# Kernel optimization log

Hardware: AMD Instinct MI355X
Metric: run time of the kernel (lower is better)

## Reference

```python
import jax, jax.numpy as jnp
import numpy as np

E, K, D, H = 8, 2, 1024, 2048   # num_experts, top_k, dim, ffn_dim
B, S = 1, 1024                   # batch, seq


def setup_inputs() -> dict:
    key = jax.random.key(0)
    k0, k1, k2, k3, k4 = jax.random.split(key, 5)
    sD = 1.0 / np.sqrt(D)
    sH = 1.0 / np.sqrt(H)
    return {
        "hidden_states": jax.random.normal(k0, (B, S, D), jnp.float32),
        "gate_w": jax.random.normal(k1, (E, D), jnp.float32) * sD,
        "w1": jax.random.normal(k2, (E, D, H), jnp.float32) * sD,
        "w2": jax.random.normal(k3, (E, H, D), jnp.float32) * sH,
        "w3": jax.random.normal(k4, (E, D, H), jnp.float32) * sD,
    }


def _grouped_swiglu(x_sorted, counts, w1, w2, w3):
    """Grouped expert SwiGLU over tokens sorted by expert id.

    x_sorted: [T, D] tokens grouped contiguously by expert (expert 0 first).
    counts:   [E] number of tokens per expert (sums to T).
    """
    if hasattr(jax.lax, "ragged_dot"):
        gs = counts.astype(jnp.int32)
        h = jax.nn.silu(jax.lax.ragged_dot(x_sorted, w1, gs)) * jax.lax.ragged_dot(x_sorted, w3, gs)
        return jax.lax.ragged_dot(h, w2, gs)
    # Fallback: per-expert masked GEMM (same math; zeros pass through silu*mul).
    pos = jnp.arange(x_sorted.shape[0])
    eid = jnp.searchsorted(jnp.cumsum(counts), pos, side="right")  # expert of each sorted token
    out = jnp.zeros((x_sorted.shape[0], w2.shape[-1]), x_sorted.dtype)
    for e in range(w1.shape[0]):
        xm = jnp.where((eid == e)[:, None], x_sorted, 0.0)
        he = jax.nn.silu(xm @ w1[e]) * (xm @ w3[e])
        out = out + he @ w2[e]
    return out


def reference(hidden_states, gate_w, w1, w2, w3):
    x = hidden_states.reshape(-1, D)                      # [N, D]
    N = x.shape[0]
    # --- router: softmax over experts, then top-k ---
    scores = jax.nn.softmax(x @ gate_w.T, axis=-1)        # [N, E]
    top_scores, sel = jax.lax.top_k(scores, K)            # [N, K]
    # flatten slot-major so flat_idx % N == token id (matches `% num_tokens`)
    sel_flat = sel.T.reshape(-1)                          # [K*N]
    scores_flat = top_scores.T.reshape(-1)                # [K*N]
    # --- reorder: stable sort by expert id ---
    order = jnp.argsort(sel_flat, stable=True)            # [K*N]
    tok_sorted = order % N                                # original token per routed slot
    scores_sorted = scores_flat[order]
    counts = jnp.bincount(sel_flat, length=E)             # tokens per expert
    # --- dispatch (ep_size=1: all-to-all is identity) + grouped expert GEMM ---
    x_sorted = x[tok_sorted]                              # [K*N, D]
    y = _grouped_swiglu(x_sorted, counts, w1, w2, w3)     # [K*N, D]
    # --- weighted scatter-combine ---
    weighted = y * scores_sorted[:, None]
    out = jnp.zeros((N, D), x.dtype).at[tok_sorted].add(weighted)
    return out.reshape(hidden_states.shape)
```

## Files before the change

### kernel.cpp

```cpp
#include <hip/hip_runtime.h>
#include <hip/hip_bf16.h>
#include <math.h>

#define NE 8
#define DD 1024
#define HH 2048
#define NTOK 1024
#define NSLOT 2048
#define NSLOTP 3072

typedef short short8v __attribute__((ext_vector_type(8)));
typedef float f32x4 __attribute__((ext_vector_type(4)));

static __device__ __forceinline__ unsigned short f2bf(float f) {
  union { __hip_bfloat16 h; unsigned short u; } c;
  c.h = __float2bfloat16(f);
  return c.u;
}

static __device__ __forceinline__ int sigma(int n) {
  return ((n >> 1) & 3) ^ ((n >> 3) & 1);
}

static __device__ __forceinline__ short8v pk8(const float* q) {
  short8v v;
#pragma unroll
  for (int i = 0; i < 8; ++i) v[i] = (short)f2bf(q[i]);
  return v;
}

__global__ __launch_bounds__(64) void krouter(const float* __restrict__ x,
                                              const float* __restrict__ gw,
                                              int* __restrict__ e_sel,
                                              float* __restrict__ w_sel) {
  int n = blockIdx.x;
  int lane = threadIdx.x;
  const float4* xr = (const float4*)(x + (size_t)n * DD);
  const float4* gr = (const float4*)gw;
  float acc[NE];
#pragma unroll
  for (int e = 0; e < NE; ++e) acc[e] = 0.f;
#pragma unroll
  for (int i = 0; i < 4; ++i) {
    float4 xv = xr[lane + i * 64];
#pragma unroll
    for (int e = 0; e < NE; ++e) {
      float4 gv = gr[e * 256 + lane + i * 64];
      acc[e] += xv.x * gv.x + xv.y * gv.y + xv.z * gv.z + xv.w * gv.w;
    }
  }
#pragma unroll
  for (int e = 0; e < NE; ++e)
#pragma unroll
    for (int off = 32; off > 0; off >>= 1) acc[e] += __shfl_xor(acc[e], off);
  if (lane == 0) {
    float m = acc[0];
#pragma unroll
    for (int e = 1; e < NE; ++e) m = fmaxf(m, acc[e]);
    float p[NE];
    float z = 0.f;
#pragma unroll
    for (int e = 0; e < NE; ++e) { p[e] = expf(acc[e] - m); z += p[e]; }
    float inv = 1.f / z;
    int e1 = 0;
#pragma unroll
    for (int e = 1; e < NE; ++e) if (acc[e] > acc[e1]) e1 = e;
    int e2 = (e1 == 0) ? 1 : 0;
#pragma unroll
    for (int e = 0; e < NE; ++e) if (e != e1 && acc[e] > acc[e2]) e2 = e;
    e_sel[n] = e1;         w_sel[n] = p[e1] * inv;
    e_sel[NTOK + n] = e2;  w_sel[NTOK + n] = p[e2] * inv;
  }
}

__global__ __launch_bounds__(256) void kbuild(const int* __restrict__ e_sel,
                                              const float* __restrict__ w_sel,
                                              int* __restrict__ tok,
                                              float* __restrict__ wgt,
                                              int* __restrict__ meta) {
  __shared__ int sc[NE], scur[NE];
  int t = threadIdx.x;
  if (t < NE) sc[t] = 0;
  __syncthreads();
  for (int s = t; s < NSLOTP; s += 256) tok[s] = -1;
  for (int s = t; s < NSLOT; s += 256) atomicAdd(&sc[e_sel[s]], 1);
  __syncthreads();
  if (t == 0) {
    int run = 0, i64 = 0, i128 = 0;
    for (int e = 0; e < NE; ++e) {
      meta[8 + e] = run; scur[e] = run;
      meta[e] = sc[e];
      int nm = (sc[e] + 127) >> 7;
      for (int m = 0; m < nm; ++m) {
        meta[128 + i128] = e; meta[152 + i128] = m; ++i128;
      }
      for (int m = 0; m < 2 * nm; ++m) {
        meta[32 + i64] = e; meta[80 + i64] = m; ++i64;
      }
      run += nm << 7;
    }
    meta[16] = i64; meta[17] = i128;
  }
  __syncthreads();
  for (int s = t; s < NSLOT; s += 256) {
    int e = e_sel[s];
    int pos = atomicAdd(&scur[e], 1);
    tok[pos] = s & (NTOK - 1);
    wgt[pos] = w_sel[s];
  }
}

__global__ __launch_bounds__(256) void kgather(const float* __restrict__ x,
                                               const int* __restrict__ tok,
                                               unsigned short* __restrict__ xg) {
  int tid = threadIdx.x;
  int row = blockIdx.x * 2 + (tid >> 7);
  int g = tid & 127;
  int t = tok[row];
  int pos = (g & 3) ^ ((row >> 1) & 3);
  char* dst = (char*)xg + (size_t)row * 2048 + (g >> 2) * 64 + (pos << 4);
  short8v v = {0, 0, 0, 0, 0, 0, 0, 0};
  if (t >= 0) {
    const float* src = x + (size_t)t * DD + g * 8;
    float q[8];
#pragma unroll
    for (int i = 0; i < 8; ++i) q[i] = src[i];
    v = pk8(q);
  }
  *(short8v*)dst = v;
}

__global__ __launch_bounds__(256, 3) void kgemm13(
    const unsigned short* __restrict__ xg, const float* __restrict__ w1,
    const float* __restrict__ w3, unsigned short* __restrict__ hws,
    const int* __restrict__ meta) {
  __shared__ __align__(16) char smem[16384];
  char* ldsB = smem;
  int vt = blockIdx.y;
  if (vt >= meta[17]) return;
  int e = meta[128 + vt], mt = meta[152 + vt];
  int n0 = blockIdx.x * 64;
  int abase = meta[8 + e] + mt * 128;
  int tid = threadIdx.x, l = tid & 63, w = tid >> 6;
  int wm = w & 1, wn = w >> 1;

  int bn = tid & 63, kb = tid >> 6;
  const float* pb1 = w1 + (size_t)e * DD * HH + (size_t)(kb * 8) * HH + n0 + bn;
  const float* pb3 = w3 + (size_t)e * DD * HH + (size_t)(kb * 8) * HH + n0 + bn;
  int wb = bn * 64 + (((kb ^ sigma(bn)) & 3) << 4);

  const char* pa[4];
#pragma unroll
  for (int mf = 0; mf < 4; ++mf) {
    int r = wm * 64 + mf * 16 + (l & 15);
    pa[mf] = (const char*)xg + (size_t)(abase + r) * 2048 +
             ((((l >> 4) ^ (r >> 1)) & 3) << 4);
  }
  int boff[2];
#pragma unroll
  for (int nf = 0; nf < 2; ++nf) {
    int n = wn * 32 + nf * 16 + (l & 15);
    boff[nf] = n * 64 + ((((l >> 4) ^ sigma(n)) & 3) << 4);
  }

  f32x4 accg[4][2], accu[4][2];
#pragma unroll
  for (int i = 0; i < 4; ++i)
#pragma unroll
    for (int j = 0; j < 2; ++j) {
      accg[i][j] = (f32x4){0.f, 0.f, 0.f, 0.f};
      accu[i][j] = (f32x4){0.f, 0.f, 0.f, 0.f};
    }

  float q1[2][8], q3[2][8];
  short8v a[4];
#pragma unroll
  for (int r = 0; r < 8; ++r) {
    q1[0][r] = pb1[(size_t)r * HH];
    q3[0][r] = pb3[(size_t)r * HH];
    q1[1][r] = pb1[(size_t)(32 + r) * HH];
    q3[1][r] = pb3[(size_t)(32 + r) * HH];
  }
#pragma unroll
  for (int mf = 0; mf < 4; ++mf) a[mf] = *(const short8v*)(pa[mf]);
  *(short8v*)(ldsB + wb) = pk8(q1[0]);
  *(short8v*)(ldsB + 4096 + wb) = pk8(q3[0]);
#pragma unroll
  for (int r = 0; r < 8; ++r) {
    q1[0][r] = pb1[(size_t)(64 + r) * HH];
    q3[0][r] = pb3[(size_t)(64 + r) * HH];
  }
  __syncthreads();

#define STEP13(S, P)                                                           \
  {                                                                            \
    if ((S) < 31) {                                                            \
      char* d = ldsB + (((P) ^ 1) << 13);                                      \
      *(short8v*)(d + wb) = pk8(q1[(P) ^ 1]);                                  \
      *(short8v*)(d + 4096 + wb) = pk8(q3[(P) ^ 1]);                           \
    }                                                                          \
    if ((S) < 29) {                                                            \
      const float* s1 = pb1 + (size_t)((S) + 3) * 32 * HH;                     \
      const float* s3 = pb3 + (size_t)((S) + 3) * 32 * HH;                     \
      _Pragma("unroll") for (int r = 0; r < 8; ++r) {                          \
        q1[(P) ^ 1][r] = s1[(size_t)r * HH];                                   \
        q3[(P) ^ 1][r] = s3[(size_t)r * HH];                                   \
      }                                                                        \
    }                                                                          \
    short8v b1f[2], b3f[2];                                                    \
    _Pragma("unroll") for (int nf = 0; nf < 2; ++nf) {                         \
      b1f[nf] = *(const short8v*)(ldsB + ((P) << 13) + boff[nf]);              \
      b3f[nf] = *(const short8v*)(ldsB + ((P) << 13) + 4096 + boff[nf]);       \
    }                                                                          \
    _Pragma("unroll") for (int nf = 0; nf < 2; ++nf)                           \
        _Pragma("unroll") for (int mf = 0; mf < 4; ++mf) {                     \
      accg[mf][nf] = __builtin_amdgcn_mfma_f32_16x16x32_bf16(                  \
          a[mf], b1f[nf], accg[mf][nf], 0, 0, 0);                              \
      accu[mf][nf] = __builtin_amdgcn_mfma_f32_16x16x32_bf16(                  \
          a[mf], b3f[nf], accu[mf][nf], 0, 0, 0);                              \
    }                                                                          \
    if ((S) < 31) {                                                           \
      _Pragma("unroll") for (int mf = 0; mf < 4; ++mf)                         \
          a[mf] = *(const short8v*)(pa[mf] + ((S) + 1) * 64);                  \
    }                                                                          \
    __syncthreads();                                                           \
  }

  for (int ss = 0; ss < 16; ++ss) {
    int s0 = 2 * ss;
    STEP13(s0, 0);
    STEP13(s0 + 1, 1);
  }
#undef STEP13

  unsigned short* hl = (unsigned short*)smem;
#pragma unroll
  for (int mf = 0; mf < 4; ++mf)
#pragma unroll
    for (int nf = 0; nf < 2; ++nf)
#pragma unroll
      for (int rr = 0; rr < 4; ++rr) {
        int row = wm * 64 + mf * 16 + ((l >> 4) << 2) + rr;
        int col = wn * 32 + nf * 16 + (l & 15);
        float gv = accg[mf][nf][rr], uv = accu[mf][nf][rr];
        hl[row * 64 + col] = f2bf((gv / (1.f + __expf(-gv))) * uv);
      }
  __syncthreads();
#pragma unroll
  for (int p = 0; p < 4; ++p) {
    int idx = p * 256 + tid;
    int row = idx >> 3, g = idx & 7;
    int dp = abase + row;
    size_t db = (size_t)dp * 4096 + (size_t)n0 * 2 + (g >> 2) * 64 +
                ((size_t)((g & 3) ^ ((dp >> 1) & 3)) << 4);
    *(short8v*)((char*)hws + db) =
        *(const short8v*)((const char*)hl + row * 128 + (g << 4));
  }
}

__global__ __launch_bounds__(256, 4) void kgemm2(
    const unsigned short* __restrict__ hws, const float* __restrict__ w2,
    float* __restrict__ out, const int* __restrict__ tok,
    const float* __restrict__ wgt, const int* __restrict__ meta) {
  __shared__ __align__(16) char smem[8192];
  char* ldsB = smem;
  int vt = blockIdx.y;
  if (vt >= meta[17]) return;
  int e = meta[128 + vt], mt = meta[152 + vt];
  int n0 = blockIdx.x * 64;
  int kz = blockIdx.z;
  int mbase = meta[8 + e] + mt * 128;
  int rem = meta[e] - mt * 128;
  int tid = threadIdx.x, l = tid & 63, w = tid >> 6;
  int wm = w & 1, wn = w >> 1;

  int bn = tid & 63, kb = tid >> 6;
  const float* pb = w2 + (size_t)e * HH * DD +
                    (size_t)(kz * 1024 + kb * 8) * DD + n0 + bn;
  int wb = bn * 64 + (((kb ^ sigma(bn)) & 3) << 4);

  const char* pa[4];
#pragma unroll
  for (int mf = 0; mf < 4; ++mf) {
    int r = wm * 64 + mf * 16 + (l & 15);
    pa[mf] = (const char*)hws + (size_t)(mbase + r) * 4096 + kz * 2048 +
             ((((l >> 4) ^ (r >> 1)) & 3) << 4);
  }
  int boff[2];
#pragma unroll
  for (int nf = 0; nf < 2; ++nf) {
    int n = wn * 32 + nf * 16 + (l & 15);
    boff[nf] = n * 64 + ((((l >> 4) ^ sigma(n)) & 3) << 4);
  }

  f32x4 acc[4][2];
#pragma unroll
  for (int i = 0; i < 4; ++i)
#pragma unroll
    for (int j = 0; j < 2; ++j) acc[i][j] = (f32x4){0.f, 0.f, 0.f, 0.f};

  float q[2][8];
  short8v a[4];
#pragma unroll
  for (int r = 0; r < 8; ++r) {
    q[0][r] = pb[(size_t)r * DD];
    q[1][r] = pb[(size_t)(32 + r) * DD];
  }
#pragma unroll
  for (int mf = 0; mf < 4; ++mf) a[mf] = *(const short8v*)(pa[mf]);
  *(short8v*)(ldsB + wb) = pk8(q[0]);
#pragma unroll
  for (int r = 0; r < 8; ++r) q[0][r] = pb[(size_t)(64 + r) * DD];
  __syncthreads();

#define STEP2(S, P)                                                            \
  {                                                                            \
    if ((S) < 31) {                                                            \
      *(short8v*)(ldsB + (((P) ^ 1) << 12) + wb) = pk8(q[(P) ^ 1]);            \
    }                                                                          \
    if ((S) < 29) {                                                            \
      const float* sp = pb + (size_t)((S) + 3) * 32 * DD;                      \
      _Pragma("unroll") for (int r = 0; r < 8; ++r)                            \
          q[(P) ^ 1][r] = sp[(size_t)r * DD];                                  \
    }                                                                          \
    short8v bf[2];                                                             \
    _Pragma("unroll") for (int nf = 0; nf < 2; ++nf)                           \
        bf[nf] = *(const short8v*)(ldsB + ((P) << 12) + boff[nf]);             \
    _Pragma("unroll") for (int nf = 0; nf < 2; ++nf)                           \
        _Pragma("unroll") for (int mf = 0; mf < 4; ++mf)                       \
            acc[mf][nf] = __builtin_amdgcn_mfma_f32_16x16x32_bf16(             \
                a[mf], bf[nf], acc[mf][nf], 0, 0, 0);                          \
    if ((S) < 31) {                                                           \
      _Pragma("unroll") for (int mf = 0; mf < 4; ++mf)                         \
          a[mf] = *(const short8v*)(pa[mf] + ((S) + 1) * 64);                  \
    }                                                                          \
    __syncthreads();                                                           \
  }

  for (int ss = 0; ss < 16; ++ss) {
    int s0 = 2 * ss;
    STEP2(s0, 0);
    STEP2(s0 + 1, 1);
  }
#undef STEP2

#pragma unroll
  for (int mf = 0; mf < 4; ++mf)
#pragma unroll
    for (int rr = 0; rr < 4; ++rr) {
      int row = wm * 64 + mf * 16 + ((l >> 4) << 2) + rr;
      if (row < rem) {
        int t = tok[mbase + row];
        float wt = wgt[mbase + row];
#pragma unroll
        for (int nf = 0; nf < 2; ++nf)
          atomicAdd(out + (size_t)t * DD + n0 + wn * 32 + nf * 16 + (l & 15),
                    wt * acc[mf][nf][rr]);
      }
    }
}

extern "C" void kernel_launch(void* const* d_in, const int* in_sizes, int n_in,
                              void* d_out, int out_size, void* d_ws, size_t ws_size,
                              hipStream_t stream) {
  const float* x  = (const float*)d_in[0];
  const float* gw = (const float*)d_in[1];
  const float* w1 = (const float*)d_in[2];
  const float* w2 = (const float*)d_in[3];
  const float* w3 = (const float*)d_in[4];
  float* out = (float*)d_out;
  char* ws = (char*)d_ws;
  const size_t MB = 1024 * 1024;
  if (ws_size < 24 * MB) return;

  unsigned short* xg  = (unsigned short*)(ws);
  unsigned short* hws = (unsigned short*)(ws + 6 * MB);
  char* mb = ws + 20 * MB;
  int*   e_sel  = (int*)mb;
  float* w_sel  = (float*)(mb + 8192);
  int*   tok    = (int*)(mb + 16384);
  float* wgt    = (float*)(mb + 16384 + 12288);
  int*   meta   = (int*)(mb + 16384 + 24576);

  hipMemsetAsync(out, 0, (size_t)out_size * sizeof(float), stream);
  krouter<<<dim3(NTOK), 64, 0, stream>>>(x, gw, e_sel, w_sel);
  kbuild<<<1, 256, 0, stream>>>(e_sel, w_sel, tok, wgt, meta);
  kgather<<<dim3(NSLOTP / 2), 256, 0, stream>>>(x, tok, xg);
  kgemm13<<<dim3(32, 24), 256, 0, stream>>>(xg, w1, w3, hws, meta);
  kgemm2<<<dim3(16, 24, 2), 256, 0, stream>>>(hws, w2, out, tok, wgt, meta);
}
```

Measured before the change: 119.4 us.

## Load expert weights directly into registers per wave, dropping LDS staging and barriers

Both expert GEMM kernels stop staging the fp32 weight tiles in shared memory. Each wave now loads its own 16-column slice straight into registers, converts it to bf16 and feeds the MFMAs with a register double buffer, so the per-step __syncthreads disappears. Each wave covers all 128 rows of the tile, and the activation XOR swizzle is removed from the gather and intermediate buffers. The cost is that every wave reloads all A rows (twice the A traffic per wave), register pressure goes up so occupancy is lowered to 2 blocks, and prefetch depth drops to one step.

```diff
diff --git a/kernel.cpp b/kernel.cpp
--- a/kernel.cpp
+++ b/kernel.cpp
@@ -16,10 +16,6 @@
   union { __hip_bfloat16 h; unsigned short u; } c;
   c.h = __float2bfloat16(f);
   return c.u;
-}
-
-static __device__ __forceinline__ int sigma(int n) {
-  return ((n >> 1) & 3) ^ ((n >> 3) & 1);
 }
 
 static __device__ __forceinline__ short8v pk8(const float* q) {
@@ -117,8 +113,7 @@
   int row = blockIdx.x * 2 + (tid >> 7);
   int g = tid & 127;
   int t = tok[row];
-  int pos = (g & 3) ^ ((row >> 1) & 3);
-  char* dst = (char*)xg + (size_t)row * 2048 + (g >> 2) * 64 + (pos << 4);
+  char* dst = (char*)xg + (size_t)row * 2048 + (g << 4);
   short8v v = {0, 0, 0, 0, 0, 0, 0, 0};
   if (t >= 0) {
     const float* src = x + (size_t)t * DD + g * 8;
@@ -130,140 +125,97 @@
   *(short8v*)dst = v;
 }
 
-__global__ __launch_bounds__(256, 3) void kgemm13(
+__global__ __launch_bounds__(256, 2) void kgemm13(
     const unsigned short* __restrict__ xg, const float* __restrict__ w1,
     const float* __restrict__ w3, unsigned short* __restrict__ hws,
     const int* __restrict__ meta) {
   __shared__ __align__(16) char smem[16384];
-  char* ldsB = smem;
   int vt = blockIdx.y;
   if (vt >= meta[17]) return;
   int e = meta[128 + vt], mt = meta[152 + vt];
   int n0 = blockIdx.x * 64;
   int abase = meta[8 + e] + mt * 128;
   int tid = threadIdx.x, l = tid & 63, w = tid >> 6;
-  int wm = w & 1, wn = w >> 1;
-
-  int bn = tid & 63, kb = tid >> 6;
-  const float* pb1 = w1 + (size_t)e * DD * HH + (size_t)(kb * 8) * HH + n0 + bn;
-  const float* pb3 = w3 + (size_t)e * DD * HH + (size_t)(kb * 8) * HH + n0 + bn;
-  int wb = bn * 64 + (((kb ^ sigma(bn)) & 3) << 4);
-
-  const char* pa[4];
-#pragma unroll
-  for (int mf = 0; mf < 4; ++mf) {
-    int r = wm * 64 + mf * 16 + (l & 15);
-    pa[mf] = (const char*)xg + (size_t)(abase + r) * 2048 +
-             ((((l >> 4) ^ (r >> 1)) & 3) << 4);
-  }
-  int boff[2];
-#pragma unroll
-  for (int nf = 0; nf < 2; ++nf) {
-    int n = wn * 32 + nf * 16 + (l & 15);
-    boff[nf] = n * 64 + ((((l >> 4) ^ sigma(n)) & 3) << 4);
-  }
-
-  f32x4 accg[4][2], accu[4][2];
-#pragma unroll
-  for (int i = 0; i < 4; ++i)
-#pragma unroll
-    for (int j = 0; j < 2; ++j) {
-      accg[i][j] = (f32x4){0.f, 0.f, 0.f, 0.f};
-      accu[i][j] = (f32x4){0.f, 0.f, 0.f, 0.f};
-    }
-
-  float q1[2][8], q3[2][8];
-  short8v a[4];
-#pragma unroll
-  for (int r = 0; r < 8; ++r) {
-    q1[0][r] = pb1[(size_t)r * HH];
-    q3[0][r] = pb3[(size_t)r * HH];
-    q1[1][r] = pb1[(size_t)(32 + r) * HH];
-    q3[1][r] = pb3[(size_t)(32 + r) * HH];
-  }
-#pragma unroll
-  for (int mf = 0; mf < 4; ++mf) a[mf] = *(const short8v*)(pa[mf]);
-  *(short8v*)(ldsB + wb) = pk8(q1[0]);
-  *(short8v*)(ldsB + 4096 + wb) = pk8(q3[0]);
-#pragma unroll
-  for (int r = 0; r < 8; ++r) {
-    q1[0][r] = pb1[(size_t)(64 + r) * HH];
-    q3[0][r] = pb3[(size_t)(64 + r) * HH];
-  }
-  __syncthreads();
-
-#define STEP13(S, P)                                                           \
+
+  const char* pa[8];
+#pragma unroll
+  for (int mf = 0; mf < 8; ++mf) {
+    int r = mf * 16 + (l & 15);
+    pa[mf] = (const char*)xg + (size_t)(abase + r) * 2048 + ((l >> 4) << 4);
+  }
+  int ncol = n0 + w * 16 + (l & 15);
+  const float* pb1 = w1 + (size_t)e * DD * HH + (size_t)((l >> 4) * 8) * HH + ncol;
+  const float* pb3 = w3 + (size_t)e * DD * HH + (size_t)((l >> 4) * 8) * HH + ncol;
+
+  f32x4 accg[8], accu[8];
+#pragma unroll
+  for (int i = 0; i < 8; ++i) {
+    accg[i] = (f32x4){0.f, 0.f, 0.f, 0.f};
+    accu[i] = (f32x4){0.f, 0.f, 0.f, 0.f};
+  }
+
+  float q1A[8], q3A[8], q1B[8], q3B[8];
+  short8v aA[8], aB[8];
+#pragma unroll
+  for (int j = 0; j < 8; ++j) {
+    q1A[j] = pb1[(size_t)j * HH];
+    q3A[j] = pb3[(size_t)j * HH];
+  }
+#pragma unroll
+  for (int mf = 0; mf < 8; ++mf) aA[mf] = *(const short8v*)(pa[mf]);
+
+#define STEP13(S, QC1, QC3, AC, QN1, QN3, AN)                                  \
   {                                                                            \
     if ((S) < 31) {                                                            \
-      char* d = ldsB + (((P) ^ 1) << 13);                                      \
-      *(short8v*)(d + wb) = pk8(q1[(P) ^ 1]);                                  \
-      *(short8v*)(d + 4096 + wb) = pk8(q3[(P) ^ 1]);                           \
+      size_t ko = (size_t)((S) + 1) * 32 * HH;                                 \
+      _Pragma("unroll") for (int j = 0; j < 8; ++j) {                          \
+        QN1[j] = pb1[ko + (size_t)j * HH];                                     \
+        QN3[j] = pb3[ko + (size_t)j * HH];                                     \
+      }                                                                        \
+      _Pragma("unroll") for (int mf = 0; mf < 8; ++mf)                         \
+          AN[mf] = *(const short8v*)(pa[mf] + ((S) + 1) * 64);                 \
     }                                                                          \
-    if ((S) < 29) {                                                            \
-      const float* s1 = pb1 + (size_t)((S) + 3) * 32 * HH;                     \
-      const float* s3 = pb3 + (size_t)((S) + 3) * 32 * HH;                     \
-      _Pragma("unroll") for (int r = 0; r < 8; ++r) {                          \
-        q1[(P) ^ 1][r] = s1[(size_t)r * HH];                                   \
-        q3[(P) ^ 1][r] = s3[(size_t)r * HH];                                   \
-      }                                                                        \
+    short8v b1 = pk8(QC1), b3 = pk8(QC3);                                      \
+    _Pragma("unroll") for (int mf = 0; mf < 8; ++mf) {                         \
+      accg[mf] = __builtin_amdgcn_mfma_f32_16x16x32_bf16(AC[mf], b1,           \
+                                                         accg[mf], 0, 0, 0);   \
+      accu[mf] = __builtin_amdgcn_mfma_f32_16x16x32_bf16(AC[mf], b3,           \
+                                                         accu[mf], 0, 0, 0);   \
     }                                                                          \
-    short8v b1f[2], b3f[2];                                                    \
-    _Pragma("unroll") for (int nf = 0; nf < 2; ++nf) {                         \
-      b1f[nf] = *(const short8v*)(ldsB + ((P) << 13) + boff[nf]);              \
-      b3f[nf] = *(const short8v*)(ldsB + ((P) << 13) + 4096 + boff[nf]);       \
-    }                                                                          \
-    _Pragma("unroll") for (int nf = 0; nf < 2; ++nf)                           \
-        _Pragma("unroll") for (int mf = 0; mf < 4; ++mf) {                     \
-      accg[mf][nf] = __builtin_amdgcn_mfma_f32_16x16x32_bf16(                  \
-          a[mf], b1f[nf], accg[mf][nf], 0, 0, 0);                              \
-      accu[mf][nf] = __builtin_amdgcn_mfma_f32_16x16x32_bf16(                  \
-          a[mf], b3f[nf], accu[mf][nf], 0, 0, 0);                              \
-    }                                                                          \
-    if ((S) < 31) {                                                           \
-      _Pragma("unroll") for (int mf = 0; mf < 4; ++mf)                         \
-          a[mf] = *(const short8v*)(pa[mf] + ((S) + 1) * 64);                  \
-    }                                                                          \
-    __syncthreads();                                                           \
   }
 
   for (int ss = 0; ss < 16; ++ss) {
     int s0 = 2 * ss;
-    STEP13(s0, 0);
-    STEP13(s0 + 1, 1);
+    STEP13(s0, q1A, q3A, aA, q1B, q3B, aB);
+    STEP13(s0 + 1, q1B, q3B, aB, q1A, q3A, aA);
   }
 #undef STEP13
 
   unsigned short* hl = (unsigned short*)smem;
 #pragma unroll
-  for (int mf = 0; mf < 4; ++mf)
-#pragma unroll
-    for (int nf = 0; nf < 2; ++nf)
-#pragma unroll
-      for (int rr = 0; rr < 4; ++rr) {
-        int row = wm * 64 + mf * 16 + ((l >> 4) << 2) + rr;
-        int col = wn * 32 + nf * 16 + (l & 15);
-        float gv = accg[mf][nf][rr], uv = accu[mf][nf][rr];
-        hl[row * 64 + col] = f2bf((gv / (1.f + __expf(-gv))) * uv);
-      }
+  for (int mf = 0; mf < 8; ++mf)
+#pragma unroll
+    for (int rr = 0; rr < 4; ++rr) {
+      int row = mf * 16 + ((l >> 4) << 2) + rr;
+      int col = w * 16 + (l & 15);
+      float gv = accg[mf][rr], uv = accu[mf][rr];
+      hl[row * 64 + col] = f2bf((gv / (1.f + __expf(-gv))) * uv);
+    }
   __syncthreads();
 #pragma unroll
   for (int p = 0; p < 4; ++p) {
     int idx = p * 256 + tid;
     int row = idx >> 3, g = idx & 7;
     int dp = abase + row;
-    size_t db = (size_t)dp * 4096 + (size_t)n0 * 2 + (g >> 2) * 64 +
-                ((size_t)((g & 3) ^ ((dp >> 1) & 3)) << 4);
-    *(short8v*)((char*)hws + db) =
+    *(short8v*)((char*)hws + (size_t)dp * 4096 + (size_t)n0 * 2 + (g << 4)) =
         *(const short8v*)((const char*)hl + row * 128 + (g << 4));
   }
 }
 
-__global__ __launch_bounds__(256, 4) void kgemm2(
+__global__ __launch_bounds__(256, 2) void kgemm2(
     const unsigned short* __restrict__ hws, const float* __restrict__ w2,
     float* __restrict__ out, const int* __restrict__ tok,
     const float* __restrict__ wgt, const int* __restrict__ meta) {
-  __shared__ __align__(16) char smem[8192];
-  char* ldsB = smem;
   int vt = blockIdx.y;
   if (vt >= meta[17]) return;
   int e = meta[128 + vt], mt = meta[152 + vt];
@@ -272,90 +224,60 @@
   int mbase = meta[8 + e] + mt * 128;
   int rem = meta[e] - mt * 128;
   int tid = threadIdx.x, l = tid & 63, w = tid >> 6;
-  int wm = w & 1, wn = w >> 1;
-
-  int bn = tid & 63, kb = tid >> 6;
+
+  const char* pa[8];
+#pragma unroll
+  for (int mf = 0; mf < 8; ++mf) {
+    int r = mf * 16 + (l & 15);
+    pa[mf] = (const char*)hws + (size_t)(mbase + r) * 4096 + kz * 2048 +
+             ((l >> 4) << 4);
+  }
+  int ncol = n0 + w * 16 + (l & 15);
   const float* pb = w2 + (size_t)e * HH * DD +
-                    (size_t)(kz * 1024 + kb * 8) * DD + n0 + bn;
-  int wb = bn * 64 + (((kb ^ sigma(bn)) & 3) << 4);
-
-  const char* pa[4];
-#pragma unroll
-  for (int mf = 0; mf < 4; ++mf) {
-    int r = wm * 64 + mf * 16 + (l & 15);
-    pa[mf] = (const char*)hws + (size_t)(mbase + r) * 4096 + kz * 2048 +
-             ((((l >> 4) ^ (r >> 1)) & 3) << 4);
-  }
-  int boff[2];
-#pragma unroll
-  for (int nf = 0; nf < 2; ++nf) {
-    int n = wn * 32 + nf * 16 + (l & 15);
-    boff[nf] = n * 64 + ((((l >> 4) ^ sigma(n)) & 3) << 4);
-  }
-
-  f32x4 acc[4][2];
-#pragma unroll
-  for (int i = 0; i < 4; ++i)
-#pragma unroll
-    for (int j = 0; j < 2; ++j) acc[i][j] = (f32x4){0.f, 0.f, 0.f, 0.f};
-
-  float q[2][8];
-  short8v a[4];
-#pragma unroll
-  for (int r = 0; r < 8; ++r) {
-    q[0][r] = pb[(size_t)r * DD];
-    q[1][r] = pb[(size_t)(32 + r) * DD];
-  }
-#pragma unroll
-  for (int mf = 0; mf < 4; ++mf) a[mf] = *(const short8v*)(pa[mf]);
-  *(short8v*)(ldsB + wb) = pk8(q[0]);
-#pragma unroll
-  for (int r = 0; r < 8; ++r) q[0][r] = pb[(size_t)(64 + r) * DD];
-  __syncthreads();
-
-#define STEP2(S, P)                                                            \
+                    (size_t)(kz * 1024 + (l >> 4) * 8) * DD + ncol;
+
+  f32x4 acc[8];
+#pragma unroll
+  for (int i = 0; i < 8; ++i) acc[i] = (f32x4){0.f, 0.f, 0.f, 0.f};
+
+  float qA[8], qB[8];
+  short8v aA[8], aB[8];
+#pragma unroll
+  for (int j = 0; j < 8; ++j) qA[j] = pb[(size_t)j * DD];
+#pragma unroll
+  for (int mf = 0; mf < 8; ++mf) aA[mf] = *(const short8v*)(pa[mf]);
+
+#define STEP2(S, QC, AC, QN, AN)                                               \
   {                                                                            \
     if ((S) < 31) {                                                            \
-      *(short8v*)(ldsB + (((P) ^ 1) << 12) + wb) = pk8(q[(P) ^ 1]);            \
+      size_t ko = (size_t)((S) + 1) * 32 * DD;                                 \
+      _Pragma("unroll") for (int j = 0; j < 8; ++j)                            \
+          QN[j] = pb[ko + (size_t)j * DD];                                     \
+      _Pragma("unroll") for (int mf = 0; mf < 8; ++mf)                         \
+          AN[mf] = *(const short8v*)(pa[mf] + ((S) + 1) * 64);                 \
     }                                                                          \
-    if ((S) < 29) {                                                            \
-      const float* sp = pb + (size_t)((S) + 3) * 32 * DD;                      \
-      _Pragma("unroll") for (int r = 0; r < 8; ++r)                            \
-          q[(P) ^ 1][r] = sp[(size_t)r * DD];                                  \
-    }                                                                          \
-    short8v bf[2];                                                             \
-    _Pragma("unroll") for (int nf = 0; nf < 2; ++nf)                           \
-        bf[nf] = *(const short8v*)(ldsB + ((P) << 12) + boff[nf]);             \
-    _Pragma("unroll") for (int nf = 0; nf < 2; ++nf)                           \
-        _Pragma("unroll") for (int mf = 0; mf < 4; ++mf)                       \
-            acc[mf][nf] = __builtin_amdgcn_mfma_f32_16x16x32_bf16(             \
-                a[mf], bf[nf], acc[mf][nf], 0, 0, 0);                          \
-    if ((S) < 31) {                                                           \
-      _Pragma("unroll") for (int mf = 0; mf < 4; ++mf)                         \
-          a[mf] = *(const short8v*)(pa[mf] + ((S) + 1) * 64);                  \
-    }                                                                          \
-    __syncthreads();                                                           \
+    short8v b = pk8(QC);                                                       \
+    _Pragma("unroll") for (int mf = 0; mf < 8; ++mf)                           \
+        acc[mf] = __builtin_amdgcn_mfma_f32_16x16x32_bf16(AC[mf], b,           \
+                                                          acc[mf], 0, 0, 0);   \
   }
 
   for (int ss = 0; ss < 16; ++ss) {
     int s0 = 2 * ss;
-    STEP2(s0, 0);
-    STEP2(s0 + 1, 1);
+    STEP2(s0, qA, aA, qB, aB);
+    STEP2(s0 + 1, qB, aB, qA, aA);
   }
 #undef STEP2
 
 #pragma unroll
-  for (int mf = 0; mf < 4; ++mf)
+  for (int mf = 0; mf < 8; ++mf)
 #pragma unroll
     for (int rr = 0; rr < 4; ++rr) {
-      int row = wm * 64 + mf * 16 + ((l >> 4) << 2) + rr;
+      int row = mf * 16 + ((l >> 4) << 2) + rr;
       if (row < rem) {
         int t = tok[mbase + row];
         float wt = wgt[mbase + row];
-#pragma unroll
-        for (int nf = 0; nf < 2; ++nf)
-          atomicAdd(out + (size_t)t * DD + n0 + wn * 32 + nf * 16 + (l & 15),
-                    wt * acc[mf][nf][rr]);
+        atomicAdd(out + (size_t)t * DD + ncol, wt * acc[mf][rr]);
       }
     }
 }
```

Result: slower. 238.5 us (+99.7%).

## Triple-buffer weight prefetch registers and double-buffer A fragments in expert GEMMs

Applied to the files above, without the earlier changes.

Restructures the main loops of both expert GEMM kernels so they use three rotating register sets for weight prefetch and two for A fragments. LDS writes for the next stage move after the MFMAs and are followed by a single waitcnt+barrier, which lets global loads, LDS stores and matrix math overlap more. It also removes the XOR swizzle from the gathered activation and intermediate layouts so those reads are linear, and simplifies the B swizzle. Register pressure rises, so launch-bounds occupancy hints are lowered, which may reduce latency hiding. The unswizzled A reads may also cost more global or cache bandwidth.

```diff
diff --git a/kernel.cpp b/kernel.cpp
--- a/kernel.cpp
+++ b/kernel.cpp
@@ -18,15 +18,17 @@
   return c.u;
 }
 
-static __device__ __forceinline__ int sigma(int n) {
-  return ((n >> 1) & 3) ^ ((n >> 3) & 1);
-}
-
 static __device__ __forceinline__ short8v pk8(const float* q) {
   short8v v;
 #pragma unroll
   for (int i = 0; i < 8; ++i) v[i] = (short)f2bf(q[i]);
   return v;
+}
+
+static __device__ __forceinline__ void barrier_lds() {
+  asm volatile("s_waitcnt lgkmcnt(0)" ::: "memory");
+  __builtin_amdgcn_s_barrier();
+  asm volatile("" ::: "memory");
 }
 
 __global__ __launch_bounds__(64) void krouter(const float* __restrict__ x,
@@ -117,8 +119,7 @@
   int row = blockIdx.x * 2 + (tid >> 7);
   int g = tid & 127;
   int t = tok[row];
-  int pos = (g & 3) ^ ((row >> 1) & 3);
-  char* dst = (char*)xg + (size_t)row * 2048 + (g >> 2) * 64 + (pos << 4);
+  char* dst = (char*)xg + (size_t)row * 2048 + (g << 4);
   short8v v = {0, 0, 0, 0, 0, 0, 0, 0};
   if (t >= 0) {
     const float* src = x + (size_t)t * DD + g * 8;
@@ -130,7 +131,7 @@
   *(short8v*)dst = v;
 }
 
-__global__ __launch_bounds__(256, 3) void kgemm13(
+__global__ __launch_bounds__(256, 2) void kgemm13(
     const unsigned short* __restrict__ xg, const float* __restrict__ w1,
     const float* __restrict__ w3, unsigned short* __restrict__ hws,
     const int* __restrict__ meta) {
@@ -147,20 +148,19 @@
   int bn = tid & 63, kb = tid >> 6;
   const float* pb1 = w1 + (size_t)e * DD * HH + (size_t)(kb * 8) * HH + n0 + bn;
   const float* pb3 = w3 + (size_t)e * DD * HH + (size_t)(kb * 8) * HH + n0 + bn;
-  int wb = bn * 64 + (((kb ^ sigma(bn)) & 3) << 4);
+  int wbB = bn * 64 + (((kb ^ (bn >> 1)) & 3) << 4);
 
   const char* pa[4];
 #pragma unroll
   for (int mf = 0; mf < 4; ++mf) {
     int r = wm * 64 + mf * 16 + (l & 15);
-    pa[mf] = (const char*)xg + (size_t)(abase + r) * 2048 +
-             ((((l >> 4) ^ (r >> 1)) & 3) << 4);
-  }
-  int boff[2];
+    pa[mf] = (const char*)xg + (size_t)(abase + r) * 2048 + ((l >> 4) << 4);
+  }
+  int bfo[2];
 #pragma unroll
   for (int nf = 0; nf < 2; ++nf) {
     int n = wn * 32 + nf * 16 + (l & 15);
-    boff[nf] = n * 64 + ((((l >> 4) ^ sigma(n)) & 3) << 4);
+    bfo[nf] = n * 64 + ((((l >> 4) ^ (n >> 1)) & 3) << 4);
   }
 
   f32x4 accg[4][2], accu[4][2];
@@ -172,67 +172,67 @@
       accu[i][j] = (f32x4){0.f, 0.f, 0.f, 0.f};
     }
 
-  float q1[2][8], q3[2][8];
-  short8v a[4];
-#pragma unroll
-  for (int r = 0; r < 8; ++r) {
-    q1[0][r] = pb1[(size_t)r * HH];
-    q3[0][r] = pb3[(size_t)r * HH];
-    q1[1][r] = pb1[(size_t)(32 + r) * HH];
-    q3[1][r] = pb3[(size_t)(32 + r) * HH];
-  }
-#pragma unroll
-  for (int mf = 0; mf < 4; ++mf) a[mf] = *(const short8v*)(pa[mf]);
-  *(short8v*)(ldsB + wb) = pk8(q1[0]);
-  *(short8v*)(ldsB + 4096 + wb) = pk8(q3[0]);
-#pragma unroll
-  for (int r = 0; r < 8; ++r) {
-    q1[0][r] = pb1[(size_t)(64 + r) * HH];
-    q3[0][r] = pb3[(size_t)(64 + r) * HH];
-  }
-  __syncthreads();
-
-#define STEP13(S, P)                                                           \
+  float q1_0[8], q3_0[8], q1_1[8], q3_1[8], q1_2[8], q3_2[8];
+  short8v aA[4], aB[4];
+#pragma unroll
+  for (int mf = 0; mf < 4; ++mf) aA[mf] = *(const short8v*)(pa[mf]);
+#pragma unroll
+  for (int j = 0; j < 8; ++j) {
+    q1_0[j] = pb1[(size_t)j * HH];          q3_0[j] = pb3[(size_t)j * HH];
+    q1_1[j] = pb1[(size_t)(32 + j) * HH];   q3_1[j] = pb3[(size_t)(32 + j) * HH];
+    q1_2[j] = pb1[(size_t)(64 + j) * HH];   q3_2[j] = pb3[(size_t)(64 + j) * HH];
+  }
+  *(short8v*)(ldsB + wbB) = pk8(q1_0);
+  *(short8v*)(ldsB + 4096 + wbB) = pk8(q3_0);
+  barrier_lds();
+
+#define STEP13(S, BUF, QW1, QW3, QN1, QN3, AC, AN, WR)                         \
   {                                                                            \
-    if ((S) < 31) {                                                            \
-      char* d = ldsB + (((P) ^ 1) << 13);                                      \
-      *(short8v*)(d + wb) = pk8(q1[(P) ^ 1]);                                  \
-      *(short8v*)(d + 4096 + wb) = pk8(q3[(P) ^ 1]);                           \
-    }                                                                          \
-    if ((S) < 29) {                                                            \
-      const float* s1 = pb1 + (size_t)((S) + 3) * 32 * HH;                     \
-      const float* s3 = pb3 + (size_t)((S) + 3) * 32 * HH;                     \
-      _Pragma("unroll") for (int r = 0; r < 8; ++r) {                          \
-        q1[(P) ^ 1][r] = s1[(size_t)r * HH];                                   \
-        q3[(P) ^ 1][r] = s3[(size_t)r * HH];                                   \
-      }                                                                        \
-    }                                                                          \
     short8v b1f[2], b3f[2];                                                    \
     _Pragma("unroll") for (int nf = 0; nf < 2; ++nf) {                         \
-      b1f[nf] = *(const short8v*)(ldsB + ((P) << 13) + boff[nf]);              \
-      b3f[nf] = *(const short8v*)(ldsB + ((P) << 13) + 4096 + boff[nf]);       \
+      b1f[nf] = *(const short8v*)(ldsB + (BUF) * 8192 + bfo[nf]);              \
+      b3f[nf] = *(const short8v*)(ldsB + (BUF) * 8192 + 4096 + bfo[nf]);       \
+    }                                                                          \
+    if (WR) {                                                                  \
+      _Pragma("unroll") for (int mf = 0; mf < 4; ++mf)                         \
+          AN[mf] = *(const short8v*)(pa[mf] + ((S) + 1) * 64);                 \
+    }                                                                          \
+    if ((S) <= 28) {                                                           \
+      size_t ko = (size_t)((S) + 3) * 32 * HH;                                 \
+      _Pragma("unroll") for (int j = 0; j < 8; ++j) {                          \
+        QN1[j] = pb1[ko + (size_t)j * HH];                                     \
+        QN3[j] = pb3[ko + (size_t)j * HH];                                     \
+      }                                                                        \
     }                                                                          \
     _Pragma("unroll") for (int nf = 0; nf < 2; ++nf)                           \
         _Pragma("unroll") for (int mf = 0; mf < 4; ++mf) {                     \
       accg[mf][nf] = __builtin_amdgcn_mfma_f32_16x16x32_bf16(                  \
-          a[mf], b1f[nf], accg[mf][nf], 0, 0, 0);                              \
+          AC[mf], b1f[nf], accg[mf][nf], 0, 0, 0);                             \
       accu[mf][nf] = __builtin_amdgcn_mfma_f32_16x16x32_bf16(                  \
-          a[mf], b3f[nf], accu[mf][nf], 0, 0, 0);                              \
-    }                                                                          \
-    if ((S) < 31) {                                                           \
-      _Pragma("unroll") for (int mf = 0; mf < 4; ++mf)                         \
-          a[mf] = *(const short8v*)(pa[mf] + ((S) + 1) * 64);                  \
-    }                                                                          \
-    __syncthreads();                                                           \
-  }
-
-  for (int ss = 0; ss < 16; ++ss) {
-    int s0 = 2 * ss;
-    STEP13(s0, 0);
-    STEP13(s0 + 1, 1);
-  }
+          AC[mf], b3f[nf], accu[mf][nf], 0, 0, 0);                             \
+    }                                                                          \
+    if (WR) {                                                                  \
+      char* d = ldsB + (((BUF) ^ 1) * 8192);                                   \
+      *(short8v*)(d + wbB) = pk8(QW1);                                         \
+      *(short8v*)(d + 4096 + wbB) = pk8(QW3);                                  \
+      barrier_lds();                                                           \
+    }                                                                          \
+  }
+
+  for (int ss = 0; ss < 5; ++ss) {
+    int s0 = 6 * ss;
+    STEP13(s0 + 0, 0, q1_1, q3_1, q1_0, q3_0, aA, aB, 1);
+    STEP13(s0 + 1, 1, q1_2, q3_2, q1_1, q3_1, aB, aA, 1);
+    STEP13(s0 + 2, 0, q1_0, q3_0, q1_2, q3_2, aA, aB, 1);
+    STEP13(s0 + 3, 1, q1_1, q3_1, q1_0, q3_0, aB, aA, 1);
+    STEP13(s0 + 4, 0, q1_2, q3_2, q1_1, q3_1, aA, aB, 1);
+    STEP13(s0 + 5, 1, q1_0, q3_0, q1_2, q3_2, aB, aA, 1);
+  }
+  STEP13(30, 0, q1_1, q3_1, q1_0, q3_0, aA, aB, 1);
+  STEP13(31, 1, q1_2, q3_2, q1_0, q3_0, aB, aA, 0);
 #undef STEP13
 
+  __syncthreads();
   unsigned short* hl = (unsigned short*)smem;
 #pragma unroll
   for (int mf = 0; mf < 4; ++mf)
@@ -251,14 +251,12 @@
     int idx = p * 256 + tid;
     int row = idx >> 3, g = idx & 7;
     int dp = abase + row;
-    size_t db = (size_t)dp * 4096 + (size_t)n0 * 2 + (g >> 2) * 64 +
-                ((size_t)((g & 3) ^ ((dp >> 1) & 3)) << 4);
-    *(short8v*)((char*)hws + db) =
+    *(short8v*)((char*)hws + (size_t)dp * 4096 + (size_t)n0 * 2 + (g << 4)) =
         *(const short8v*)((const char*)hl + row * 128 + (g << 4));
   }
 }
 
-__global__ __launch_bounds__(256, 4) void kgemm2(
+__global__ __launch_bounds__(256, 3) void kgemm2(
     const unsigned short* __restrict__ hws, const float* __restrict__ w2,
     float* __restrict__ out, const int* __restrict__ tok,
     const float* __restrict__ wgt, const int* __restrict__ meta) {
@@ -277,20 +275,20 @@
   int bn = tid & 63, kb = tid >> 6;
   const float* pb = w2 + (size_t)e * HH * DD +
                     (size_t)(kz * 1024 + kb * 8) * DD + n0 + bn;
-  int wb = bn * 64 + (((kb ^ sigma(bn)) & 3) << 4);
+  int wbB = bn * 64 + (((kb ^ (bn >> 1)) & 3) << 4);
 
   const char* pa[4];
 #pragma unroll
   for (int mf = 0; mf < 4; ++mf) {
     int r = wm * 64 + mf * 16 + (l & 15);
     pa[mf] = (const char*)hws + (size_t)(mbase + r) * 4096 + kz * 2048 +
-             ((((l >> 4) ^ (r >> 1)) & 3) << 4);
-  }
-  int boff[2];
+             ((l >> 4) << 4);
+  }
+  int bfo[2];
 #pragma unroll
   for (int nf = 0; nf < 2; ++nf) {
     int n = wn * 32 + nf * 16 + (l & 15);
-    boff[nf] = n * 64 + ((((l >> 4) ^ sigma(n)) & 3) << 4);
+    bfo[nf] = n * 64 + ((((l >> 4) ^ (n >> 1)) & 3) << 4);
   }
 
   f32x4 acc[4][2];
@@ -299,49 +297,54 @@
 #pragma unroll
     for (int j = 0; j < 2; ++j) acc[i][j] = (f32x4){0.f, 0.f, 0.f, 0.f};
 
-  float q[2][8];
-  short8v a[4];
-#pragma unroll
-  for (int r = 0; r < 8; ++r) {
-    q[0][r] = pb[(size_t)r * DD];
-    q[1][r] = pb[(size_t)(32 + r) * DD];
-  }
-#pragma unroll
-  for (int mf = 0; mf < 4; ++mf) a[mf] = *(const short8v*)(pa[mf]);
-  *(short8v*)(ldsB + wb) = pk8(q[0]);
-#pragma unroll
-  for (int r = 0; r < 8; ++r) q[0][r] = pb[(size_t)(64 + r) * DD];
-  __syncthreads();
-
-#define STEP2(S, P)                                                            \
+  float q_0[8], q_1[8], q_2[8];
+  short8v aA[4], aB[4];
+#pragma unroll
+  for (int mf = 0; mf < 4; ++mf) aA[mf] = *(const short8v*)(pa[mf]);
+#pragma unroll
+  for (int j = 0; j < 8; ++j) {
+    q_0[j] = pb[(size_t)j * DD];
+    q_1[j] = pb[(size_t)(32 + j) * DD];
+    q_2[j] = pb[(size_t)(64 + j) * DD];
+  }
+  *(short8v*)(ldsB + wbB) = pk8(q_0);
+  barrier_lds();
+
+#define STEP2(S, BUF, QW, QN, AC, AN, WR)                                      \
   {                                                                            \
-    if ((S) < 31) {                                                            \
-      *(short8v*)(ldsB + (((P) ^ 1) << 12) + wb) = pk8(q[(P) ^ 1]);            \
-    }                                                                          \
-    if ((S) < 29) {                                                            \
-      const float* sp = pb + (size_t)((S) + 3) * 32 * DD;                      \
-      _Pragma("unroll") for (int r = 0; r < 8; ++r)                            \
-          q[(P) ^ 1][r] = sp[(size_t)r * DD];                                  \
-    }                                                                          \
     short8v bf[2];                                                             \
     _Pragma("unroll") for (int nf = 0; nf < 2; ++nf)                           \
-        bf[nf] = *(const short8v*)(ldsB + ((P) << 12) + boff[nf]);             \
+        bf[nf] = *(const short8v*)(ldsB + (BUF) * 4096 + bfo[nf]);             \
+    if (WR) {                                                                  \
+      _Pragma("unroll") for (int mf = 0; mf < 4; ++mf)                         \
+          AN[mf] = *(const short8v*)(pa[mf] + ((S) + 1) * 64);                 \
+    }                                                                          \
+    if ((S) <= 28) {                                                           \
+      size_t ko = (size_t)((S) + 3) * 32 * DD;                                 \
+      _Pragma("unroll") for (int j = 0; j < 8; ++j)                            \
+          QN[j] = pb[ko + (size_t)j * DD];                                     \
+    }                                                                          \
     _Pragma("unroll") for (int nf = 0; nf < 2; ++nf)                           \
         _Pragma("unroll") for (int mf = 0; mf < 4; ++mf)                       \
             acc[mf][nf] = __builtin_amdgcn_mfma_f32_16x16x32_bf16(             \
-                a[mf], bf[nf], acc[mf][nf], 0, 0, 0);                          \
-    if ((S) < 31) {                                                           \
-      _Pragma("unroll") for (int mf = 0; mf < 4; ++mf)                         \
-          a[mf] = *(const short8v*)(pa[mf] + ((S) + 1) * 64);                  \
-    }                                                                          \
-    __syncthreads();                                                           \
-  }
-
-  for (int ss = 0; ss < 16; ++ss) {
-    int s0 = 2 * ss;
-    STEP2(s0, 0);
-    STEP2(s0 + 1, 1);
-  }
+                AC[mf], bf[nf], acc[mf][nf], 0, 0, 0);                         \
+    if (WR) {                                                                  \
+      *(short8v*)(ldsB + (((BUF) ^ 1) * 4096) + wbB) = pk8(QW);                \
+      barrier_lds();                                                           \
+    }                                                                          \
+  }
+
+  for (int ss = 0; ss < 5; ++ss) {
+    int s0 = 6 * ss;
+    STEP2(s0 + 0, 0, q_1, q_0, aA, aB, 1);
+    STEP2(s0 + 1, 1, q_2, q_1, aB, aA, 1);
+    STEP2(s0 + 2, 0, q_0, q_2, aA, aB, 1);
+    STEP2(s0 + 3, 1, q_1, q_0, aB, aA, 1);
+    STEP2(s0 + 4, 0, q_2, q_1, aA, aB, 1);
+    STEP2(s0 + 5, 1, q_0, q_2, aB, aA, 1);
+  }
+  STEP2(30, 0, q_1, q_0, aA, aB, 1);
+  STEP2(31, 1, q_2, q_0, aB, aA, 0);
 #undef STEP2
 
 #pragma unroll
```

New measurement: 149.0 us. 24.7% more time.
